# Kernel optimization log

Hardware: AMD Instinct MI355X
Metric: run time of the kernel (lower is better)

## Reference

```python
import jax, jax.numpy as jnp
import numpy as np

N_EMBEDDING = 32
HEAD_SIZE = 64
B, T = 8, 4096


def setup_inputs() -> dict:
    key = jax.random.key(0)
    kx, kk, kq, kv = jax.random.split(key, 4)
    x = jax.random.normal(kx, (B, T, N_EMBEDDING), dtype=jnp.float32)
    Wk = jax.random.normal(kk, (N_EMBEDDING, HEAD_SIZE), dtype=jnp.float32) * 0.05
    Wq = jax.random.normal(kq, (N_EMBEDDING, HEAD_SIZE), dtype=jnp.float32) * 0.05
    Wv = jax.random.normal(kv, (N_EMBEDDING, HEAD_SIZE), dtype=jnp.float32) * 0.05
    return {"x": x, "Wk": Wk, "Wq": Wq, "Wv": Wv}


def reference(x, Wk, Wq, Wv):
    # x: [B, T, C]; projections (no bias)
    k = jnp.einsum("btc,cd->btd", x, Wk)  # [B,T,D]
    q = jnp.einsum("btc,cd->btd", x, Wq)
    v = jnp.einsum("btc,cd->btd", x, Wv)
    # raw scores (NOTE: original module applies no 1/sqrt(D) scaling)
    wei = jnp.einsum("bqd,bkd->bqk", q, k)  # [B,T,T]
    t = x.shape[1]
    causal = jnp.tril(jnp.ones((t, t), dtype=bool))
    wei = jnp.where(causal[None, :, :], wei, -jnp.inf)
    wei = jax.nn.softmax(wei, axis=-1)
    out = jnp.einsum("bqk,bkd->bqd", wei, v)  # [B,T,D]
    return out
```

## Files before the change

kernel.cpp:

```cpp
#include <hip/hip_runtime.h>
#include <hip/hip_bf16.h>

constexpr int Bc = 8;
constexpr int Tt = 4096;
constexpr int Dd = 64;

typedef __attribute__((ext_vector_type(8))) short short8;
typedef __attribute__((ext_vector_type(4))) float floatx4;
typedef uint4   __attribute__((may_alias)) uint4_a;
typedef short8  __attribute__((may_alias)) short8_a;
typedef ushort4 __attribute__((may_alias)) ushort4_a;
typedef float4  __attribute__((may_alias)) float4_a;

#define MFMA16(A, B, C) __builtin_amdgcn_mfma_f32_16x16x32_bf16(A, B, C, 0, 0, 0)
constexpr float LOG2E = 1.4426950408889634f;

__device__ __forceinline__ unsigned rnd16(float x) {
    unsigned u; __builtin_memcpy(&u, &x, 4); return u + 0x8000u;
}
__device__ __forceinline__ unsigned pk_bf2(float lo, float hi) {
    return __builtin_amdgcn_perm(rnd16(hi), rnd16(lo), 0x07060302);
}
__device__ __forceinline__ ushort4 pack4(floatx4 d) {
    union { unsigned u[2]; ushort4 v; } r;
    r.u[0] = pk_bf2(d[0], d[1]);
    r.u[1] = pk_bf2(d[2], d[3]);
    return r.v;
}
__device__ __forceinline__ short8 cvt8(float4 a, float4 b) {
    union { unsigned u[4]; short8 s; } r;
    r.u[0] = pk_bf2(a.x, a.y);
    r.u[1] = pk_bf2(a.z, a.w);
    r.u[2] = pk_bf2(b.x, b.y);
    r.u[3] = pk_bf2(b.z, b.w);
    return r.s;
}

__global__ __launch_bounds__(512, 4) void attn_kernel(
    const float* __restrict__ x,
    const float* __restrict__ Wk, const float* __restrict__ Wq,
    const float* __restrict__ Wv,
    float* __restrict__ out)
{
    __shared__ uint4 sK[1024];
    __shared__ uint4 sVt[1024];
    __shared__ uint4 sP[1024];

    int b   = blockIdx.x & 7;
    int idx = blockIdx.x >> 3;
    int qt  = (idx < 32) ? (63 - idx) : (idx - 32);
    int q0 = qt * 64;
    int tid  = threadIdx.x;
    int wave = tid >> 6, lane = tid & 63;
    int group = wave >> 2, gw = wave & 3;
    int ln15 = lane & 15, quad = lane >> 4;
    size_t bT = (size_t)b * Tt;
    int qrow = q0 + gw*16 + ln15;

    short8 wk_f[4], wv_f[4];
    #pragma unroll
    for (int c = 0; c < 4; ++c) {
        int col = 16*c + ln15;
        union { unsigned u[4]; short8 s; } rk, rv;
        #pragma unroll
        for (int jj = 0; jj < 4; ++jj) {
            const float* k0 = Wk + (quad*8 + 2*jj) * 64 + col;
            const float* v0 = Wv + (quad*8 + 2*jj) * 64 + col;
            rk.u[jj] = pk_bf2(k0[0], k0[64]);
            rv.u[jj] = pk_bf2(v0[0], v0[64]);
        }
        wk_f[c] = rk.s; wv_f[c] = rv.s;
    }

    {
        int qt_w = wave >> 1, dbase = (wave & 1) * 2;
        const float* xp = x + (bT + q0 + qt_w*16 + ln15)*32 + quad*8;
        float4 x0 = ((const float4_a*)xp)[0];
        float4 x1 = ((const float4_a*)xp)[1];
        short8 xq = cvt8(x0, x1);
        unsigned short* sQh = (unsigned short*)sP;
        int ql = qt_w*16 + ln15;
        #pragma unroll
        for (int i = 0; i < 2; ++i) {
            int dt = dbase + i;
            int col = 16*dt + ln15;
            union { unsigned u[4]; short8 s; } rq;
            #pragma unroll
            for (int jj = 0; jj < 4; ++jj) {
                const float* q0p = Wq + (quad*8 + 2*jj) * 64 + col;
                rq.u[jj] = pk_bf2(q0p[0] * LOG2E, q0p[64] * LOG2E);
            }
            floatx4 d = (floatx4){0.f, 0.f, 0.f, 0.f};
            d = MFMA16(rq.s, xq, d);
            int graw = 2*dt + (quad >> 1);
            *(ushort4_a*)(sQh + ql*64 + ((graw ^ (ql & 7)) << 3)
                              + ((quad & 1) << 2)) = pack4(d);
        }
    }
    __syncthreads();
    short8 bq0, bq1;
    {
        int ql = gw*16 + ln15;
        union { uint4 u; short8 s; } t0, t1;
        t0.u = sP[ql*8 + (quad ^ (ql & 7))];
        t1.u = sP[ql*8 + ((quad + 4) ^ (ql & 7))];
        bq0 = t0.s; bq1 = t1.s;
    }

    floatx4 o4[4];
    #pragma unroll
    for (int c = 0; c < 4; ++c) o4[c] = (floatx4){0.f, 0.f, 0.f, 0.f};
    float l_lane = 0.f;

    const int sbase   = group * 512;
    const int sbase_h = group * 4096;
    const int nIter = qt/2 + 1;
    unsigned short* sKh = (unsigned short*)sK;
    unsigned short* sVh = (unsigned short*)sVt;

    float4 pX0 = {0,0,0,0}, pX1 = {0,0,0,0};
    if (group <= qt) {
        const float* xp = x + (bT + group*64 + 16*gw + ln15)*32 + quad*8;
        pX0 = ((const float4_a*)xp)[0];
        pX1 = ((const float4_a*)xp)[1];
    }

    for (int it = 0; it < nIter; ++it) {
        int kt = 2*it + group;
        bool active = (kt <= qt);
        __syncthreads();
        if (active) {
            short8 xf = cvt8(pX0, pX1);
            int key = 16*gw + ln15;
            #pragma unroll
            for (int c = 0; c < 4; ++c) {
                floatx4 dk = (floatx4){0.f, 0.f, 0.f, 0.f};
                dk = MFMA16(wk_f[c], xf, dk);
                int g1 = 2*c + (quad >> 1);
                *(ushort4_a*)(sKh + sbase_h + key*64 + ((g1 ^ (key & 7)) << 3)
                                  + ((quad & 1) << 2)) = pack4(dk);
                floatx4 dv = (floatx4){0.f, 0.f, 0.f, 0.f};
                dv = MFMA16(xf, wv_f[c], dv);
                int dcol = 16*c + ln15;
                int g2 = 2*gw + (quad >> 1);
                *(ushort4_a*)(sVh + sbase_h + dcol*64 + ((g2 ^ (dcol & 7)) << 3)
                                  + ((quad & 1) << 2)) = pack4(dv);
            }
        }
        int ktn = kt + 2;
        if (ktn <= qt) {
            const float* xp = x + (bT + ktn*64 + 16*gw + ln15)*32 + quad*8;
            pX0 = ((const float4_a*)xp)[0];
            pX1 = ((const float4_a*)xp)[1];
        }
        __syncthreads();
        if (!active) continue;
        int k0 = kt * 64;

        floatx4 s4[4];
        #pragma unroll
        for (int t = 0; t < 4; ++t) {
            int kr = 16*t + ln15;
            union { uint4 u; short8 s; } a0, a1;
            a0.u = sK[sbase + kr*8 + (quad ^ (ln15 & 7))];
            a1.u = sK[sbase + kr*8 + ((quad + 4) ^ (ln15 & 7))];
            floatx4 c = (floatx4){0.f, 0.f, 0.f, 0.f};
            c = MFMA16(a0.s, bq0, c);
            c = MFMA16(a1.s, bq1, c);
            s4[t] = c;
        }

        unsigned long long* sP64 = (unsigned long long*)sP;
        const int pb = wave*256 + ln15*16;
        const int xk = ln15 & 14;
        if (kt == qt) {
            #pragma unroll
            for (int t = 0; t < 4; ++t) {
                int keyb = k0 + 16*t + quad*4;
                float p[4];
                #pragma unroll
                for (int r = 0; r < 4; ++r) {
                    p[r] = (keyb + r <= qrow) ? __builtin_amdgcn_exp2f(s4[t][r]) : 0.f;
                    l_lane += p[r];
                }
                unsigned long long pk =
                    ((unsigned long long)pk_bf2(p[2], p[3]) << 32) | pk_bf2(p[0], p[1]);
                sP64[pb + ((4*t + quad) ^ xk)] = pk;
            }
        } else {
            #pragma unroll
            for (int t = 0; t < 4; ++t) {
                float p[4];
                #pragma unroll
                for (int r = 0; r < 4; ++r) {
                    p[r] = __builtin_amdgcn_exp2f(s4[t][r]);
                    l_lane += p[r];
                }
                unsigned long long pk =
                    ((unsigned long long)pk_bf2(p[2], p[3]) << 32) | pk_bf2(p[0], p[1]);
                sP64[pb + ((4*t + quad) ^ xk)] = pk;
            }
        }

        int h = (ln15 >> 1) & 7;
        union { uint4 u; short8 s; } p0, p1;
        p0.u = sP[wave*128 + ln15*8 + (quad ^ h)];
        p1.u = sP[wave*128 + ln15*8 + ((quad + 4) ^ h)];
        #pragma unroll
        for (int c = 0; c < 4; ++c) {
            int dr = 16*c + ln15;
            union { uint4 u; short8 s; } v0, v1;
            v0.u = sVt[sbase + dr*8 + (quad ^ (dr & 7))];
            v1.u = sVt[sbase + dr*8 + ((quad + 4) ^ (dr & 7))];
            o4[c] = MFMA16(v0.s, p0.s, o4[c]);
            o4[c] = MFMA16(v1.s, p1.s, o4[c]);
        }
    }

    l_lane += __shfl_xor(l_lane, 16);
    l_lane += __shfl_xor(l_lane, 32);

    __syncthreads();
    if (group == 1) {
        float4* mo = (gw < 2) ? (float4*)&sK[512 + gw*256]
                              : (float4*)&sVt[512 + (gw - 2)*256];
        #pragma unroll
        for (int c = 0; c < 4; ++c)
            mo[lane*4 + c] = make_float4(o4[c][0], o4[c][1], o4[c][2], o4[c][3]);
        ((float*)sP)[2048 + gw*64 + lane] = l_lane;
    }
    __syncthreads();
    if (group == 0) {
        float4* mo = (gw < 2) ? (float4*)&sK[512 + gw*256]
                              : (float4*)&sVt[512 + (gw - 2)*256];
        l_lane += ((float*)sP)[2048 + gw*64 + lane];
        float inv = 1.f / l_lane;
        #pragma unroll
        for (int c = 0; c < 4; ++c) {
            float4 po = mo[lane*4 + c];
            float4 res = make_float4((o4[c][0] + po.x) * inv,
                                     (o4[c][1] + po.y) * inv,
                                     (o4[c][2] + po.z) * inv,
                                     (o4[c][3] + po.w) * inv);
            *(float4*)(out + (bT + q0 + gw*16 + ln15) * Dd + 16*c + quad*4) = res;
        }
    }
}

extern "C" void kernel_launch(void* const* d_in, const int* in_sizes, int n_in,
                              void* d_out, int out_size, void* d_ws, size_t ws_size,
                              hipStream_t stream)
{
    const float* x  = (const float*)d_in[0];
    const float* Wk = (const float*)d_in[1];
    const float* Wq = (const float*)d_in[2];
    const float* Wv = (const float*)d_in[3];
    float* out = (float*)d_out;

    attn_kernel<<<Bc * (Tt / 64), 512, 0, stream>>>(x, Wk, Wq, Wv, out);
}
```

Before: 102.9 us.

## Split causal attention tile pairs evenly across blocks with atomic accumulation

```diff
diff --git a/kernel.cpp b/kernel.cpp
--- a/kernel.cpp
+++ b/kernel.cpp
@@ -4,6 +4,9 @@
 constexpr int Bc = 8;
 constexpr int Tt = 4096;
 constexpr int Dd = 64;
+constexpr int NT = 2080;
+constexpr int CPB = 8;
+constexpr int BPB = NT / CPB;
 
 typedef __attribute__((ext_vector_type(8))) short short8;
 typedef __attribute__((ext_vector_type(4))) float floatx4;
@@ -36,26 +39,36 @@
     return r.s;
 }
 
-__global__ __launch_bounds__(512, 4) void attn_kernel(
+__global__ __launch_bounds__(512) void zero_kernel(float4* __restrict__ p) {
+    p[(size_t)blockIdx.x * 512 + threadIdx.x] = make_float4(0.f, 0.f, 0.f, 0.f);
+}
+
+__global__ __launch_bounds__(256, 5) void attn_accum(
     const float* __restrict__ x,
     const float* __restrict__ Wk, const float* __restrict__ Wq,
     const float* __restrict__ Wv,
-    float* __restrict__ out)
+    float* __restrict__ Oacc, float* __restrict__ Lacc)
 {
-    __shared__ uint4 sK[1024];
-    __shared__ uint4 sVt[1024];
-    __shared__ uint4 sP[1024];
-
-    int b   = blockIdx.x & 7;
-    int idx = blockIdx.x >> 3;
-    int qt  = (idx < 32) ? (63 - idx) : (idx - 32);
-    int q0 = qt * 64;
+    __shared__ uint4 sK[512];
+    __shared__ uint4 sVt[512];
+    __shared__ uint4 sP[512];
+
+    int b = blockIdx.x / BPB;
+    int j = blockIdx.x % BPB;
+    int f0 = j * CPB;
+
+    int A = NT - f0;
+    int n = (int)((__builtin_sqrtf(8.f * (float)(A - 1) + 1.f) - 1.f) * 0.5f);
+    while (n * (n + 1) / 2 > A - 1) --n;
+    while ((n + 1) * (n + 2) / 2 <= A - 1) ++n;
+    int qt_c = n;
+    int kt_c = f0 - NT + (n + 1) * (n + 2) / 2;
+
     int tid  = threadIdx.x;
     int wave = tid >> 6, lane = tid & 63;
-    int group = wave >> 2, gw = wave & 3;
+    int gw = wave;
     int ln15 = lane & 15, quad = lane >> 4;
     size_t bT = (size_t)b * Tt;
-    int qrow = q0 + gw*16 + ln15;
 
     short8 wk_f[4], wv_f[4];
     #pragma unroll
@@ -72,64 +85,70 @@
         wk_f[c] = rk.s; wv_f[c] = rv.s;
     }
 
-    {
-        int qt_w = wave >> 1, dbase = (wave & 1) * 2;
-        const float* xp = x + (bT + q0 + qt_w*16 + ln15)*32 + quad*8;
+    short8 bq0, bq1;
+    floatx4 o4[4];
+    float l_lane;
+
+    unsigned short* sQh = (unsigned short*)sP + wave * 1024;
+    auto regenQ = [&](int qtn) {
+        const float* xp = x + (bT + qtn*64 + gw*16 + ln15) * 32 + quad*8;
         float4 x0 = ((const float4_a*)xp)[0];
         float4 x1 = ((const float4_a*)xp)[1];
         short8 xq = cvt8(x0, x1);
-        unsigned short* sQh = (unsigned short*)sP;
-        int ql = qt_w*16 + ln15;
-        #pragma unroll
-        for (int i = 0; i < 2; ++i) {
-            int dt = dbase + i;
+        #pragma unroll
+        for (int dt = 0; dt < 4; ++dt) {
             int col = 16*dt + ln15;
             union { unsigned u[4]; short8 s; } rq;
             #pragma unroll
             for (int jj = 0; jj < 4; ++jj) {
-                const float* q0p = Wq + (quad*8 + 2*jj) * 64 + col;
-                rq.u[jj] = pk_bf2(q0p[0] * LOG2E, q0p[64] * LOG2E);
+                const float* qp = Wq + (quad*8 + 2*jj) * 64 + col;
+                rq.u[jj] = pk_bf2(qp[0] * LOG2E, qp[64] * LOG2E);
             }
             floatx4 d = (floatx4){0.f, 0.f, 0.f, 0.f};
             d = MFMA16(rq.s, xq, d);
             int graw = 2*dt + (quad >> 1);
-            *(ushort4_a*)(sQh + ql*64 + ((graw ^ (ql & 7)) << 3)
+            *(ushort4_a*)(sQh + ln15*64 + ((graw ^ (ln15 & 7)) << 3)
                               + ((quad & 1) << 2)) = pack4(d);
         }
-    }
-    __syncthreads();
-    short8 bq0, bq1;
+        union { uint4 u; short8 s; } t0, t1;
+        t0.u = sP[wave*128 + ln15*8 + (quad ^ (ln15 & 7))];
+        t1.u = sP[wave*128 + ln15*8 + ((quad + 4) ^ (ln15 & 7))];
+        bq0 = t0.s; bq1 = t1.s;
+        #pragma unroll
+        for (int c = 0; c < 4; ++c) o4[c] = (floatx4){0.f, 0.f, 0.f, 0.f};
+        l_lane = 0.f;
+    };
+
+    auto flush = [&](int qtf) {
+        int q = qtf*64 + gw*16 + ln15;
+        float* Ob = Oacc + (bT + q) * 64;
+        #pragma unroll
+        for (int c = 0; c < 4; ++c)
+            #pragma unroll
+            for (int r = 0; r < 4; ++r)
+                atomicAdd(Ob + 16*c + quad*4 + r, o4[c][r]);
+        float v = l_lane;
+        v += __shfl_xor(v, 16);
+        v += __shfl_xor(v, 32);
+        if (quad == 0) atomicAdd(Lacc + bT + q, v);
+    };
+
+    regenQ(qt_c);
+
+    float4 pX0, pX1;
     {
-        int ql = gw*16 + ln15;
-        union { uint4 u; short8 s; } t0, t1;
-        t0.u = sP[ql*8 + (quad ^ (ql & 7))];
-        t1.u = sP[ql*8 + ((quad + 4) ^ (ql & 7))];
-        bq0 = t0.s; bq1 = t1.s;
-    }
-
-    floatx4 o4[4];
-    #pragma unroll
-    for (int c = 0; c < 4; ++c) o4[c] = (floatx4){0.f, 0.f, 0.f, 0.f};
-    float l_lane = 0.f;
-
-    const int sbase   = group * 512;
-    const int sbase_h = group * 4096;
-    const int nIter = qt/2 + 1;
-    unsigned short* sKh = (unsigned short*)sK;
-    unsigned short* sVh = (unsigned short*)sVt;
-
-    float4 pX0 = {0,0,0,0}, pX1 = {0,0,0,0};
-    if (group <= qt) {
-        const float* xp = x + (bT + group*64 + 16*gw + ln15)*32 + quad*8;
+        const float* xp = x + (bT + kt_c*64 + 16*gw + ln15) * 32 + quad*8;
         pX0 = ((const float4_a*)xp)[0];
         pX1 = ((const float4_a*)xp)[1];
     }
 
-    for (int it = 0; it < nIter; ++it) {
-        int kt = 2*it + group;
-        bool active = (kt <= qt);
+    unsigned short* sKh = (unsigned short*)sK;
+    unsigned short* sVh = (unsigned short*)sVt;
+    int qrow = qt_c*64 + gw*16 + ln15;
+
+    for (int it = 0; it < CPB; ++it) {
         __syncthreads();
-        if (active) {
+        {
             short8 xf = cvt8(pX0, pX1);
             int key = 16*gw + ln15;
             #pragma unroll
@@ -137,33 +156,34 @@
                 floatx4 dk = (floatx4){0.f, 0.f, 0.f, 0.f};
                 dk = MFMA16(wk_f[c], xf, dk);
                 int g1 = 2*c + (quad >> 1);
-                *(ushort4_a*)(sKh + sbase_h + key*64 + ((g1 ^ (key & 7)) << 3)
+                *(ushort4_a*)(sKh + key*64 + ((g1 ^ (key & 7)) << 3)
                                   + ((quad & 1) << 2)) = pack4(dk);
                 floatx4 dv = (floatx4){0.f, 0.f, 0.f, 0.f};
                 dv = MFMA16(xf, wv_f[c], dv);
                 int dcol = 16*c + ln15;
                 int g2 = 2*gw + (quad >> 1);
-                *(ushort4_a*)(sVh + sbase_h + dcol*64 + ((g2 ^ (dcol & 7)) << 3)
+                *(ushort4_a*)(sVh + dcol*64 + ((g2 ^ (dcol & 7)) << 3)
                                   + ((quad & 1) << 2)) = pack4(dv);
             }
         }
-        int ktn = kt + 2;
-        if (ktn <= qt) {
-            const float* xp = x + (bT + ktn*64 + 16*gw + ln15)*32 + quad*8;
+        int nq = qt_c, nk = kt_c + 1;
+        bool newq = (nk > qt_c);
+        if (newq) { nq = qt_c - 1; nk = 0; }
+        if (it < CPB - 1) {
+            const float* xp = x + (bT + nk*64 + 16*gw + ln15) * 32 + quad*8;
             pX0 = ((const float4_a*)xp)[0];
             pX1 = ((const float4_a*)xp)[1];
         }
         __syncthreads();
-        if (!active) continue;
-        int k0 = kt * 64;
+        int k0 = kt_c * 64;
 
         floatx4 s4[4];
         #pragma unroll
         for (int t = 0; t < 4; ++t) {
             int kr = 16*t + ln15;
             union { uint4 u; short8 s; } a0, a1;
-            a0.u = sK[sbase + kr*8 + (quad ^ (ln15 & 7))];
-            a1.u = sK[sbase + kr*8 + ((quad + 4) ^ (ln15 & 7))];
+            a0.u = sK[kr*8 + (quad ^ (ln15 & 7))];
+            a1.u = sK[kr*8 + ((quad + 4) ^ (ln15 & 7))];
             floatx4 c = (floatx4){0.f, 0.f, 0.f, 0.f};
             c = MFMA16(a0.s, bq0, c);
             c = MFMA16(a1.s, bq1, c);
@@ -173,7 +193,7 @@
         unsigned long long* sP64 = (unsigned long long*)sP;
         const int pb = wave*256 + ln15*16;
         const int xk = ln15 & 14;
-        if (kt == qt) {
+        if (kt_c == qt_c) {
             #pragma unroll
             for (int t = 0; t < 4; ++t) {
                 int keyb = k0 + 16*t + quad*4;
@@ -210,41 +230,31 @@
         for (int c = 0; c < 4; ++c) {
             int dr = 16*c + ln15;
             union { uint4 u; short8 s; } v0, v1;
-            v0.u = sVt[sbase + dr*8 + (quad ^ (dr & 7))];
-            v1.u = sVt[sbase + dr*8 + ((quad + 4) ^ (dr & 7))];
+            v0.u = sVt[dr*8 + (quad ^ (dr & 7))];
+            v1.u = sVt[dr*8 + ((quad + 4) ^ (dr & 7))];
             o4[c] = MFMA16(v0.s, p0.s, o4[c]);
             o4[c] = MFMA16(v1.s, p1.s, o4[c]);
         }
+
+        if (it == CPB - 1) {
+            flush(qt_c);
+        } else if (newq) {
+            flush(qt_c);
+            regenQ(nq);
+            qrow = nq*64 + gw*16 + ln15;
+        }
+        qt_c = nq; kt_c = nk;
     }
-
-    l_lane += __shfl_xor(l_lane, 16);
-    l_lane += __shfl_xor(l_lane, 32);
-
-    __syncthreads();
-    if (group == 1) {
-        float4* mo = (gw < 2) ? (float4*)&sK[512 + gw*256]
-                              : (float4*)&sVt[512 + (gw - 2)*256];
-        #pragma unroll
-        for (int c = 0; c < 4; ++c)
-            mo[lane*4 + c] = make_float4(o4[c][0], o4[c][1], o4[c][2], o4[c][3]);
-        ((float*)sP)[2048 + gw*64 + lane] = l_lane;
-    }
-    __syncthreads();
-    if (group == 0) {
-        float4* mo = (gw < 2) ? (float4*)&sK[512 + gw*256]
-                              : (float4*)&sVt[512 + (gw - 2)*256];
-        l_lane += ((float*)sP)[2048 + gw*64 + lane];
-        float inv = 1.f / l_lane;
-        #pragma unroll
-        for (int c = 0; c < 4; ++c) {
-            float4 po = mo[lane*4 + c];
-            float4 res = make_float4((o4[c][0] + po.x) * inv,
-                                     (o4[c][1] + po.y) * inv,
-                                     (o4[c][2] + po.z) * inv,
-                                     (o4[c][3] + po.w) * inv);
-            *(float4*)(out + (bT + q0 + gw*16 + ln15) * Dd + 16*c + quad*4) = res;
-        }
-    }
+}
+
+__global__ __launch_bounds__(256) void norm_kernel(
+    const float4* __restrict__ Oacc, const float* __restrict__ Lacc,
+    float4* __restrict__ out)
+{
+    int i = blockIdx.x * 256 + threadIdx.x;
+    float inv = 1.f / Lacc[i >> 4];
+    float4 o = Oacc[i];
+    out[i] = make_float4(o.x * inv, o.y * inv, o.z * inv, o.w * inv);
 }
 
 extern "C" void kernel_launch(void* const* d_in, const int* in_sizes, int n_in,
@@ -257,5 +267,10 @@
     const float* Wv = (const float*)d_in[3];
     float* out = (float*)d_out;
 
-    attn_kernel<<<Bc * (Tt / 64), 512, 0, stream>>>(x, Wk, Wq, Wv, out);
-}
+    float* Oacc = (float*)d_ws;
+    float* Lacc = Oacc + (size_t)Bc * Tt * Dd;
+
+    zero_kernel<<<1040, 512, 0, stream>>>((float4*)d_ws);
+    attn_accum<<<Bc * BPB, 256, 0, stream>>>(x, Wk, Wq, Wv, Oacc, Lacc);
+    norm_kernel<<<2048, 256, 0, stream>>>((const float4*)Oacc, Lacc, (float4*)out);
+}
```

Result: slower. 254.6 us (+147.5%).

## Pair complementary causal query tiles per 1024-thread block with four-way key split

Applied to the files above, without the earlier changes.

```diff
diff --git a/kernel.cpp b/kernel.cpp
--- a/kernel.cpp
+++ b/kernel.cpp
@@ -36,26 +36,22 @@
     return r.s;
 }
 
-__global__ __launch_bounds__(512, 4) void attn_kernel(
+__global__ __launch_bounds__(1024) void attn_kernel(
     const float* __restrict__ x,
     const float* __restrict__ Wk, const float* __restrict__ Wq,
     const float* __restrict__ Wv,
     float* __restrict__ out)
 {
-    __shared__ uint4 sK[1024];
-    __shared__ uint4 sVt[1024];
-    __shared__ uint4 sP[1024];
-
-    int b   = blockIdx.x & 7;
-    int idx = blockIdx.x >> 3;
-    int qt  = (idx < 32) ? (63 - idx) : (idx - 32);
-    int q0 = qt * 64;
+    __shared__ uint4 sStage[4096];
+    __shared__ uint4 sP[2048];
+
+    int b  = blockIdx.x & 7;
+    int pr = blockIdx.x >> 3;
     int tid  = threadIdx.x;
     int wave = tid >> 6, lane = tid & 63;
     int group = wave >> 2, gw = wave & 3;
     int ln15 = lane & 15, quad = lane >> 4;
     size_t bT = (size_t)b * Tt;
-    int qrow = q0 + gw*16 + ln15;
 
     short8 wk_f[4], wv_f[4];
     #pragma unroll
@@ -71,179 +67,186 @@
         }
         wk_f[c] = rk.s; wv_f[c] = rv.s;
     }
-
+    short8 wq_f;
     {
-        int qt_w = wave >> 1, dbase = (wave & 1) * 2;
-        const float* xp = x + (bT + q0 + qt_w*16 + ln15)*32 + quad*8;
-        float4 x0 = ((const float4_a*)xp)[0];
-        float4 x1 = ((const float4_a*)xp)[1];
-        short8 xq = cvt8(x0, x1);
-        unsigned short* sQh = (unsigned short*)sP;
-        int ql = qt_w*16 + ln15;
+        int dt = wave >> 2, colD = 16*dt + ln15;
+        union { unsigned u[4]; short8 s; } rq;
         #pragma unroll
-        for (int i = 0; i < 2; ++i) {
-            int dt = dbase + i;
-            int col = 16*dt + ln15;
-            union { unsigned u[4]; short8 s; } rq;
-            #pragma unroll
-            for (int jj = 0; jj < 4; ++jj) {
-                const float* q0p = Wq + (quad*8 + 2*jj) * 64 + col;
-                rq.u[jj] = pk_bf2(q0p[0] * LOG2E, q0p[64] * LOG2E);
-            }
+        for (int jj = 0; jj < 4; ++jj) {
+            const float* qp = Wq + (quad*8 + 2*jj) * 64 + colD;
+            rq.u[jj] = pk_bf2(qp[0] * LOG2E, qp[64] * LOG2E);
+        }
+        wq_f = rq.s;
+    }
+
+    const int stK = group * 1024;
+    const int stV = group * 1024 + 512;
+    unsigned short* sSh = (unsigned short*)sStage;
+    const int stK_h = stK * 8, stV_h = stV * 8;
+
+    #pragma unroll
+    for (int phase = 0; phase < 2; ++phase) {
+        const int qtP = (phase == 0) ? (63 - pr) : pr;
+        const int q0 = qtP * 64;
+        const int qrow = q0 + gw*16 + ln15;
+
+        {
+            int qs = wave & 3, dt = wave >> 2;
+            const float* xp = x + (bT + q0 + qs*16 + ln15)*32 + quad*8;
+            float4 x0 = ((const float4_a*)xp)[0];
+            float4 x1 = ((const float4_a*)xp)[1];
+            short8 xq = cvt8(x0, x1);
             floatx4 d = (floatx4){0.f, 0.f, 0.f, 0.f};
-            d = MFMA16(rq.s, xq, d);
+            d = MFMA16(wq_f, xq, d);
+            int ql = qs*16 + ln15;
             int graw = 2*dt + (quad >> 1);
+            unsigned short* sQh = (unsigned short*)sP;
             *(ushort4_a*)(sQh + ql*64 + ((graw ^ (ql & 7)) << 3)
                               + ((quad & 1) << 2)) = pack4(d);
         }
-    }
-    __syncthreads();
-    short8 bq0, bq1;
-    {
-        int ql = gw*16 + ln15;
-        union { uint4 u; short8 s; } t0, t1;
-        t0.u = sP[ql*8 + (quad ^ (ql & 7))];
-        t1.u = sP[ql*8 + ((quad + 4) ^ (ql & 7))];
-        bq0 = t0.s; bq1 = t1.s;
-    }
-
-    floatx4 o4[4];
-    #pragma unroll
-    for (int c = 0; c < 4; ++c) o4[c] = (floatx4){0.f, 0.f, 0.f, 0.f};
-    float l_lane = 0.f;
-
-    const int sbase   = group * 512;
-    const int sbase_h = group * 4096;
-    const int nIter = qt/2 + 1;
-    unsigned short* sKh = (unsigned short*)sK;
-    unsigned short* sVh = (unsigned short*)sVt;
-
-    float4 pX0 = {0,0,0,0}, pX1 = {0,0,0,0};
-    if (group <= qt) {
-        const float* xp = x + (bT + group*64 + 16*gw + ln15)*32 + quad*8;
-        pX0 = ((const float4_a*)xp)[0];
-        pX1 = ((const float4_a*)xp)[1];
-    }
-
-    for (int it = 0; it < nIter; ++it) {
-        int kt = 2*it + group;
-        bool active = (kt <= qt);
-        __syncthreads();
-        if (active) {
-            short8 xf = cvt8(pX0, pX1);
-            int key = 16*gw + ln15;
-            #pragma unroll
-            for (int c = 0; c < 4; ++c) {
-                floatx4 dk = (floatx4){0.f, 0.f, 0.f, 0.f};
-                dk = MFMA16(wk_f[c], xf, dk);
-                int g1 = 2*c + (quad >> 1);
-                *(ushort4_a*)(sKh + sbase_h + key*64 + ((g1 ^ (key & 7)) << 3)
-                                  + ((quad & 1) << 2)) = pack4(dk);
-                floatx4 dv = (floatx4){0.f, 0.f, 0.f, 0.f};
-                dv = MFMA16(xf, wv_f[c], dv);
-                int dcol = 16*c + ln15;
-                int g2 = 2*gw + (quad >> 1);
-                *(ushort4_a*)(sVh + sbase_h + dcol*64 + ((g2 ^ (dcol & 7)) << 3)
-                                  + ((quad & 1) << 2)) = pack4(dv);
-            }
-        }
-        int ktn = kt + 2;
-        if (ktn <= qt) {
-            const float* xp = x + (bT + ktn*64 + 16*gw + ln15)*32 + quad*8;
+        __syncthreads();
+        short8 bq0, bq1;
+        {
+            int ql = gw*16 + ln15;
+            union { uint4 u; short8 s; } t0, t1;
+            t0.u = sP[ql*8 + (quad ^ (ql & 7))];
+            t1.u = sP[ql*8 + ((quad + 4) ^ (ql & 7))];
+            bq0 = t0.s; bq1 = t1.s;
+        }
+        floatx4 o4[4];
+        #pragma unroll
+        for (int c = 0; c < 4; ++c) o4[c] = (floatx4){0.f, 0.f, 0.f, 0.f};
+        float l_lane = 0.f;
+
+        const int nIter = (qtP + 4) >> 2;
+        float4 pX0, pX1;
+        if (group <= qtP) {
+            const float* xp = x + (bT + group*64 + 16*gw + ln15)*32 + quad*8;
             pX0 = ((const float4_a*)xp)[0];
             pX1 = ((const float4_a*)xp)[1];
         }
-        __syncthreads();
-        if (!active) continue;
-        int k0 = kt * 64;
-
-        floatx4 s4[4];
-        #pragma unroll
-        for (int t = 0; t < 4; ++t) {
-            int kr = 16*t + ln15;
-            union { uint4 u; short8 s; } a0, a1;
-            a0.u = sK[sbase + kr*8 + (quad ^ (ln15 & 7))];
-            a1.u = sK[sbase + kr*8 + ((quad + 4) ^ (ln15 & 7))];
-            floatx4 c = (floatx4){0.f, 0.f, 0.f, 0.f};
-            c = MFMA16(a0.s, bq0, c);
-            c = MFMA16(a1.s, bq1, c);
-            s4[t] = c;
-        }
-
-        unsigned long long* sP64 = (unsigned long long*)sP;
-        const int pb = wave*256 + ln15*16;
-        const int xk = ln15 & 14;
-        if (kt == qt) {
+
+        for (int it = 0; it < nIter; ++it) {
+            int kt = 4*it + group;
+            bool active = (kt <= qtP);
+            __syncthreads();
+            if (active) {
+                short8 xf = cvt8(pX0, pX1);
+                int key = 16*gw + ln15;
+                #pragma unroll
+                for (int c = 0; c < 4; ++c) {
+                    floatx4 dk = (floatx4){0.f, 0.f, 0.f, 0.f};
+                    dk = MFMA16(wk_f[c], xf, dk);
+                    int g1 = 2*c + (quad >> 1);
+                    *(ushort4_a*)(sSh + stK_h + key*64 + ((g1 ^ (key & 7)) << 3)
+                                      + ((quad & 1) << 2)) = pack4(dk);
+                    floatx4 dv = (floatx4){0.f, 0.f, 0.f, 0.f};
+                    dv = MFMA16(xf, wv_f[c], dv);
+                    int dcol = 16*c + ln15;
+                    int g2 = 2*gw + (quad >> 1);
+                    *(ushort4_a*)(sSh + stV_h + dcol*64 + ((g2 ^ (dcol & 7)) << 3)
+                                      + ((quad & 1) << 2)) = pack4(dv);
+                }
+            }
+            int ktn = kt + 4;
+            if (ktn <= qtP) {
+                const float* xp = x + (bT + ktn*64 + 16*gw + ln15)*32 + quad*8;
+                pX0 = ((const float4_a*)xp)[0];
+                pX1 = ((const float4_a*)xp)[1];
+            }
+            __syncthreads();
+            if (!active) continue;
+            int k0 = kt * 64;
+
+            floatx4 s4[4];
             #pragma unroll
             for (int t = 0; t < 4; ++t) {
-                int keyb = k0 + 16*t + quad*4;
-                float p[4];
-                #pragma unroll
-                for (int r = 0; r < 4; ++r) {
-                    p[r] = (keyb + r <= qrow) ? __builtin_amdgcn_exp2f(s4[t][r]) : 0.f;
-                    l_lane += p[r];
-                }
-                unsigned long long pk =
-                    ((unsigned long long)pk_bf2(p[2], p[3]) << 32) | pk_bf2(p[0], p[1]);
-                sP64[pb + ((4*t + quad) ^ xk)] = pk;
-            }
-        } else {
-            #pragma unroll
-            for (int t = 0; t < 4; ++t) {
-                float p[4];
-                #pragma unroll
-                for (int r = 0; r < 4; ++r) {
-                    p[r] = __builtin_amdgcn_exp2f(s4[t][r]);
-                    l_lane += p[r];
-                }
-                unsigned long long pk =
-                    ((unsigned long long)pk_bf2(p[2], p[3]) << 32) | pk_bf2(p[0], p[1]);
-                sP64[pb + ((4*t + quad) ^ xk)] = pk;
-            }
-        }
-
-        int h = (ln15 >> 1) & 7;
-        union { uint4 u; short8 s; } p0, p1;
-        p0.u = sP[wave*128 + ln15*8 + (quad ^ h)];
-        p1.u = sP[wave*128 + ln15*8 + ((quad + 4) ^ h)];
-        #pragma unroll
-        for (int c = 0; c < 4; ++c) {
-            int dr = 16*c + ln15;
-            union { uint4 u; short8 s; } v0, v1;
-            v0.u = sVt[sbase + dr*8 + (quad ^ (dr & 7))];
-            v1.u = sVt[sbase + dr*8 + ((quad + 4) ^ (dr & 7))];
-            o4[c] = MFMA16(v0.s, p0.s, o4[c]);
-            o4[c] = MFMA16(v1.s, p1.s, o4[c]);
-        }
-    }
-
-    l_lane += __shfl_xor(l_lane, 16);
-    l_lane += __shfl_xor(l_lane, 32);
-
-    __syncthreads();
-    if (group == 1) {
-        float4* mo = (gw < 2) ? (float4*)&sK[512 + gw*256]
-                              : (float4*)&sVt[512 + (gw - 2)*256];
-        #pragma unroll
-        for (int c = 0; c < 4; ++c)
-            mo[lane*4 + c] = make_float4(o4[c][0], o4[c][1], o4[c][2], o4[c][3]);
-        ((float*)sP)[2048 + gw*64 + lane] = l_lane;
-    }
-    __syncthreads();
-    if (group == 0) {
-        float4* mo = (gw < 2) ? (float4*)&sK[512 + gw*256]
-                              : (float4*)&sVt[512 + (gw - 2)*256];
-        l_lane += ((float*)sP)[2048 + gw*64 + lane];
-        float inv = 1.f / l_lane;
-        #pragma unroll
-        for (int c = 0; c < 4; ++c) {
-            float4 po = mo[lane*4 + c];
-            float4 res = make_float4((o4[c][0] + po.x) * inv,
-                                     (o4[c][1] + po.y) * inv,
-                                     (o4[c][2] + po.z) * inv,
-                                     (o4[c][3] + po.w) * inv);
-            *(float4*)(out + (bT + q0 + gw*16 + ln15) * Dd + 16*c + quad*4) = res;
-        }
+                int kr = 16*t + ln15;
+                union { uint4 u; short8 s; } a0, a1;
+                a0.u = sStage[stK + kr*8 + (quad ^ (ln15 & 7))];
+                a1.u = sStage[stK + kr*8 + ((quad + 4) ^ (ln15 & 7))];
+                floatx4 c = (floatx4){0.f, 0.f, 0.f, 0.f};
+                c = MFMA16(a0.s, bq0, c);
+                c = MFMA16(a1.s, bq1, c);
+                s4[t] = c;
+            }
+
+            unsigned long long* sP64 = (unsigned long long*)sP;
+            const int pb = wave*256 + ln15*16;
+            const int xk = ln15 & 14;
+            if (kt == qtP) {
+                #pragma unroll
+                for (int t = 0; t < 4; ++t) {
+                    int keyb = k0 + 16*t + quad*4;
+                    float p[4];
+                    #pragma unroll
+                    for (int r = 0; r < 4; ++r) {
+                        p[r] = (keyb + r <= qrow) ? __builtin_amdgcn_exp2f(s4[t][r]) : 0.f;
+                        l_lane += p[r];
+                    }
+                    unsigned long long pk =
+                        ((unsigned long long)pk_bf2(p[2], p[3]) << 32) | pk_bf2(p[0], p[1]);
+                    sP64[pb + ((4*t + quad) ^ xk)] = pk;
+                }
+            } else {
+                #pragma unroll
+                for (int t = 0; t < 4; ++t) {
+                    float p[4];
+                    #pragma unroll
+                    for (int r = 0; r < 4; ++r) {
+                        p[r] = __builtin_amdgcn_exp2f(s4[t][r]);
+                        l_lane += p[r];
+                    }
+                    unsigned long long pk =
+                        ((unsigned long long)pk_bf2(p[2], p[3]) << 32) | pk_bf2(p[0], p[1]);
+                    sP64[pb + ((4*t + quad) ^ xk)] = pk;
+                }
+            }
+
+            int h = (ln15 >> 1) & 7;
+            union { uint4 u; short8 s; } p0, p1;
+            p0.u = sP[wave*128 + ln15*8 + (quad ^ h)];
+            p1.u = sP[wave*128 + ln15*8 + ((quad + 4) ^ h)];
+            #pragma unroll
+            for (int c = 0; c < 4; ++c) {
+                int dr = 16*c + ln15;
+                union { uint4 u; short8 s; } v0, v1;
+                v0.u = sStage[stV + dr*8 + (quad ^ (dr & 7))];
+                v1.u = sStage[stV + dr*8 + ((quad + 4) ^ (dr & 7))];
+                o4[c] = MFMA16(v0.s, p0.s, o4[c]);
+                o4[c] = MFMA16(v1.s, p1.s, o4[c]);
+            }
+        }
+
+        __syncthreads();
+        int li = gw*64 + lane;
+        ((float*)sP)[wave*64 + lane] = l_lane;
+        if (group != 0) {
+            float4* st = (float4*)(sStage + group*1024);
+            #pragma unroll
+            for (int c = 0; c < 4; ++c)
+                st[c*256 + li] = make_float4(o4[c][0], o4[c][1], o4[c][2], o4[c][3]);
+        }
+        __syncthreads();
+        if (group == 0) {
+            float l = l_lane + ((float*)sP)[256 + li]
+                    + ((float*)sP)[512 + li] + ((float*)sP)[768 + li];
+            l += __shfl_xor(l, 16);
+            l += __shfl_xor(l, 32);
+            float inv = 1.f / l;
+            #pragma unroll
+            for (int c = 0; c < 4; ++c) {
+                float ax = o4[c][0], ay = o4[c][1], az = o4[c][2], aw = o4[c][3];
+                #pragma unroll
+                for (int g = 1; g < 4; ++g) {
+                    float4 p = ((float4*)(sStage + g*1024))[c*256 + li];
+                    ax += p.x; ay += p.y; az += p.z; aw += p.w;
+                }
+                *(float4_a*)(out + (bT + q0 + gw*16 + ln15) * Dd + 16*c + quad*4)
+                    = make_float4(ax*inv, ay*inv, az*inv, aw*inv);
+            }
+        }
+        __syncthreads();
     }
 }
 
@@ -257,5 +260,5 @@
     const float* Wv = (const float*)d_in[3];
     float* out = (float*)d_out;
 
-    attn_kernel<<<Bc * (Tt / 64), 512, 0, stream>>>(x, Wk, Wq, Wv, out);
-}
+    attn_kernel<<<Bc * 32, 1024, 0, stream>>>(x, Wk, Wq, Wv, out);
+}
```

Result: no change. 102.9 us (-0.0%).
